# Kernel tuning notes

Hardware: AMD Instinct MI355X
Metric: run time of the kernel (lower is better)

Reference implementation:

```python
import jax, jax.numpy as jnp
import numpy as np

N_NODES = 50000
N_EDGES = 800000
IN_DIM = 128
OUT_DIM = 128
N_CLASSES = 10
N_GRAPHS = 64


def setup_inputs() -> dict:
    key = jax.random.key(0)
    ks = jax.random.split(key, 8)
    features = jax.random.normal(ks[0], (N_NODES, IN_DIM), dtype=jnp.float32)
    src = jax.random.randint(ks[1], (N_EDGES,), 0, N_NODES, dtype=jnp.int64)
    dst = jax.random.randint(ks[2], (N_EDGES,), 0, N_NODES, dtype=jnp.int64)
    graph_ids = jnp.sort(jax.random.randint(ks[3], (N_NODES,), 0, N_GRAPHS, dtype=jnp.int64))
    # GraphConv params (glorot-ish scale) and linear head params
    W = jax.random.normal(ks[4], (IN_DIM, OUT_DIM), dtype=jnp.float32) / np.sqrt(IN_DIM)
    b = jnp.zeros((OUT_DIM,), dtype=jnp.float32)
    W_head = jax.random.normal(ks[5], (OUT_DIM, N_CLASSES), dtype=jnp.float32) / np.sqrt(OUT_DIM)
    b_head = jnp.zeros((N_CLASSES,), dtype=jnp.float32)
    return {"features": features, "src": src, "dst": dst, "graph_ids": graph_ids,
            "W": W, "b": b, "W_head": W_head, "b_head": b_head}


def reference(features, src, dst, graph_ids, W, b, W_head, b_head):
    # DGL GraphConv, norm='both': D_out^-1/2 -> sum aggregate -> D_in^-1/2 -> XW+b -> relu
    ones_e = jnp.ones((src.shape[0],), dtype=features.dtype)
    out_deg = jax.ops.segment_sum(ones_e, src, num_segments=N_NODES)
    in_deg = jax.ops.segment_sum(ones_e, dst, num_segments=N_NODES)
    out_norm = jax.lax.rsqrt(jnp.clip(out_deg, 1.0))[:, None]   # [N,1]
    in_norm = jax.lax.rsqrt(jnp.clip(in_deg, 1.0))[:, None]     # [N,1]
    h = features * out_norm                                      # [N,D]
    agg = jax.ops.segment_sum(h[src], dst, num_segments=N_NODES) # gather-scatter [E,D]->[N,D]
    agg = agg * in_norm
    h = jax.nn.relu(agg @ W + b)                                 # [N,D_out]
    # dgl.mean_nodes: segment mean over graphs (note: original returns after layer 0)
    cnt = jax.ops.segment_sum(jnp.ones((N_NODES,), dtype=h.dtype), graph_ids, num_segments=N_GRAPHS)
    pooled = jax.ops.segment_sum(h, graph_ids, num_segments=N_GRAPHS) / jnp.clip(cnt, 1.0)[:, None]
    return pooled @ W_head + b_head                              # [G, n_classes]
```

## Files before the change

### kernel.cpp

```cpp
#include <hip/hip_runtime.h>

#define N_NODES   50000
#define N_EDGES   800000
#define DIM       128
#define N_GRAPHS  64
#define N_CLASSES 10
#define CAP       64
#define NCHE      64
#define CSZ       (N_EDGES / NCHE)
#define LQ        (N_NODES / 4)
#define WPB       64
#define NBR2      ((LQ + WPB - 1) / WPB)
#define PLACE_BPC ((CSZ + 255) / 256)
#define PLACE_BLKS (NCHE * PLACE_BPC)
#define PRES_BLKS ((N_NODES * DIM / 8 + 255) / 256)
#define K3_BLKS   (PLACE_BLKS + PRES_BLKS)
#define WT_BLKS   (DIM * DIM / 256)
#define GS_BLKS   ((N_NODES + 255) / 256)
#define LH_HIST   (2 * NCHE)
#define K1_BLKS   (LH_HIST + WT_BLKS + GS_BLKS)
#define NPBM      64
#define NBLK_NODE ((N_NODES + NPBM - 1) / NPBM)
#define WPAD      136

typedef _Float16 h8 __attribute__((ext_vector_type(8)));
typedef float f4v __attribute__((ext_vector_type(4)));

#define RSQN(D) rsqrtf(fmaxf((float)(D), 1.0f))

__global__ __launch_bounds__(256) void k_pre(const int* __restrict__ src,
                                             const int* __restrict__ dst,
                                             unsigned* __restrict__ Hin,
                                             unsigned* __restrict__ Hout,
                                             unsigned char* __restrict__ perm,
                                             const float* __restrict__ W,
                                             _Float16* __restrict__ Wt,
                                             const int* __restrict__ gid,
                                             int* __restrict__ gstart,
                                             const float* __restrict__ bh,
                                             float* __restrict__ out) {
    __shared__ unsigned L[LQ];
    int blk = blockIdx.x, t = threadIdx.x;
    if (blk >= LH_HIST) {
        int q = blk - LH_HIST;
        if (q < WT_BLKS) {
            int i = q * 256 + t;
            int n = i >> 7, k = i & 127;
            Wt[n * DIM + k] = (_Float16)W[k * DIM + n];
            if (i < N_GRAPHS * N_CLASSES) out[i] = bh[i % N_CLASSES];
        } else {
            int i = (q - WT_BLKS) * 256 + t;
            if (i < N_NODES) {
                int gq = gid[i];
                if (i == 0) {
                    for (int x = 0; x <= gq; ++x) gstart[x] = 0;
                } else {
                    int gp = gid[i - 1];
                    if (gp != gq)
                        for (int x = gp + 1; x <= gq; ++x) gstart[x] = i;
                }
                if (i == N_NODES - 1)
                    for (int x = gq + 1; x <= N_GRAPHS; ++x) gstart[x] = N_NODES;
            }
        }
        return;
    }
    int c = blk & (NCHE - 1);
    int phase = blk >> 6;
    int base = c * CSZ;
    for (int w = t; w < LQ; w += 256) L[w] = 0u;
    __syncthreads();
    if (phase == 0) {
        for (int i = t; i < CSZ; i += 256) {
            int d = dst[base + i];
            int sh = (d & 3) * 8;
            unsigned old = atomicAdd(&L[d >> 2], 1u << sh);
            perm[base + i] = (unsigned char)((old >> sh) & 0xffu);
        }
        __syncthreads();
        for (int w = t; w < LQ; w += 256) Hin[(size_t)c * LQ + w] = L[w];
    } else {
        for (int i = t; i < CSZ; i += 256) {
            int s = src[base + i];
            atomicAdd(&L[s >> 2], 1u << ((s & 3) * 8));
        }
        __syncthreads();
        for (int w = t; w < LQ; w += 256) Hout[(size_t)c * LQ + w] = L[w];
    }
}

__global__ __launch_bounds__(256) void k_reduce(unsigned* __restrict__ Hin,
                                                const unsigned* __restrict__ Hout,
                                                unsigned* __restrict__ indeg,
                                                unsigned* __restrict__ outdeg) {
    __shared__ unsigned sIn[4][WPB];
    __shared__ unsigned sOut[4][WPB];
    int t = threadIdx.x;
    int wl = t & (WPB - 1);
    int g  = t >> 6;
    int w  = blockIdx.x * WPB + wl;
    unsigned gs = 0, os = 0;
    int c0 = g * (NCHE / 4);
    if (w < LQ) {
        for (int c = c0; c < c0 + NCHE / 4; ++c) {
            gs += Hin[(size_t)c * LQ + w];
            os += Hout[(size_t)c * LQ + w];
        }
    }
    sIn[g][wl] = gs; sOut[g][wl] = os;
    __syncthreads();
    unsigned baseg = 0;
    for (int gg = 0; gg < 4; ++gg) if (gg < g) baseg += sIn[gg][wl];
    if (w < LQ) {
        unsigned running = baseg;
        for (int c = c0; c < c0 + NCHE / 4; ++c) {
            size_t idx = (size_t)c * LQ + w;
            unsigned word = Hin[idx];
            Hin[idx] = running;
            running += word;
        }
    }
    __syncthreads();
    if (t < WPB) {
        int ww = blockIdx.x * WPB + t;
        if (ww < LQ) {
            unsigned tot  = sIn[0][t] + sIn[1][t] + sIn[2][t] + sIn[3][t];
            unsigned otot = sOut[0][t] + sOut[1][t] + sOut[2][t] + sOut[3][t];
            int n = 4 * ww;
            indeg[n]      = tot & 0xffu;
            indeg[n + 1]  = (tot >> 8) & 0xffu;
            indeg[n + 2]  = (tot >> 16) & 0xffu;
            indeg[n + 3]  = tot >> 24;
            outdeg[n]     = otot & 0xffu;
            outdeg[n + 1] = (otot >> 8) & 0xffu;
            outdeg[n + 2] = (otot >> 16) & 0xffu;
            outdeg[n + 3] = otot >> 24;
        }
    }
}

__global__ __launch_bounds__(256) void k_place(const int* __restrict__ src,
                                               const int* __restrict__ dst,
                                               const unsigned* __restrict__ Hin,
                                               const unsigned char* __restrict__ perm,
                                               unsigned short* __restrict__ bsrc,
                                               const float* __restrict__ feat,
                                               const unsigned* __restrict__ outdeg,
                                               _Float16* __restrict__ sfeat) {
    int t = threadIdx.x;
    int blk = blockIdx.x;
    if (blk < PLACE_BLKS) {
        int c = blk / PLACE_BPC;
        int i = (blk % PLACE_BPC) * 256 + t;
        if (i < CSZ) {
            int e = c * CSZ + i;
            int d = dst[e];
            int sh = (d & 3) * 8;
            unsigned pre = (Hin[(size_t)c * LQ + (d >> 2)] >> sh) & 0xffu;
            unsigned slot = pre + perm[e];
            if (slot < CAP) bsrc[(size_t)d * CAP + slot] = (unsigned short)src[e];
        }
    } else {
        int i = (blk - PLACE_BLKS) * 256 + t;
        if (i < N_NODES * DIM / 8) {
            int n = i >> 4;
            float nrm = RSQN(outdeg[n]);
            const float4* p = reinterpret_cast<const float4*>(feat + (size_t)i * 8);
            float4 a = p[0], qv = p[1];
            h8 r;
            r[0] = (_Float16)(a.x * nrm);  r[1] = (_Float16)(a.y * nrm);
            r[2] = (_Float16)(a.z * nrm);  r[3] = (_Float16)(a.w * nrm);
            r[4] = (_Float16)(qv.x * nrm); r[5] = (_Float16)(qv.y * nrm);
            r[6] = (_Float16)(qv.z * nrm); r[7] = (_Float16)(qv.w * nrm);
            *reinterpret_cast<h8*>(sfeat + (size_t)i * 8) = r;
        }
    }
}

__device__ __forceinline__ h8 shfl_down_h8(h8 v, int d) {
    union { h8 h; int i[4]; } u;
    u.h = v;
    u.i[0] = __shfl_down(u.i[0], d);
    u.i[1] = __shfl_down(u.i[1], d);
    u.i[2] = __shfl_down(u.i[2], d);
    u.i[3] = __shfl_down(u.i[3], d);
    return u.h;
}

__global__ __launch_bounds__(256) void k_gather(const unsigned short* __restrict__ bsrc,
                                                const unsigned* __restrict__ indeg,
                                                const _Float16* __restrict__ sfeat,
                                                _Float16* __restrict__ aggh) {
    int tid = threadIdx.x;
    int wave = tid >> 6;
    int lane = tid & 63;
    int node = blockIdx.x * 4 + wave;
    if (node >= N_NODES) return;
    unsigned start = (unsigned)node * CAP;
    unsigned deg   = indeg[node];
    unsigned lim   = deg < (unsigned)CAP ? deg : (unsigned)CAP;
    int qtr = lane >> 4;
    int d8  = (lane & 15) << 3;
    int sIdx = 0;
    if ((unsigned)lane < lim) sIdx = bsrc[start + lane];
    h8 accA = (h8)(_Float16)0.f;
    h8 accC = (h8)(_Float16)0.f;
    for (unsigned j = 0; j < lim; j += 16) {
        unsigned j0 = j + qtr, j1 = j + 4 + qtr, j2 = j + 8 + qtr, j3 = j + 12 + qtr;
        int s0 = __shfl(sIdx, (int)(j0 < lim ? j0 : 0u));
        int s1 = __shfl(sIdx, (int)(j1 < lim ? j1 : 0u));
        int s2 = __shfl(sIdx, (int)(j2 < lim ? j2 : 0u));
        int s3 = __shfl(sIdx, (int)(j3 < lim ? j3 : 0u));
        _Float16 m0 = (j0 < lim) ? (_Float16)1.f : (_Float16)0.f;
        _Float16 m1 = (j1 < lim) ? (_Float16)1.f : (_Float16)0.f;
        _Float16 m2 = (j2 < lim) ? (_Float16)1.f : (_Float16)0.f;
        _Float16 m3 = (j3 < lim) ? (_Float16)1.f : (_Float16)0.f;
        h8 r0 = *reinterpret_cast<const h8*>(sfeat + (size_t)s0 * DIM + d8);
        h8 r1 = *reinterpret_cast<const h8*>(sfeat + (size_t)s1 * DIM + d8);
        h8 r2 = *reinterpret_cast<const h8*>(sfeat + (size_t)s2 * DIM + d8);
        h8 r3 = *reinterpret_cast<const h8*>(sfeat + (size_t)s3 * DIM + d8);
        accA += r0 * m0;
        accC += r1 * m1;
        accA += r2 * m2;
        accC += r3 * m3;
    }
    accA += accC;
    accA += shfl_down_h8(accA, 32);
    accA += shfl_down_h8(accA, 16);
    if (qtr == 0) {
        float innrm = RSQN(deg);
        h8 r;
#pragma unroll
        for (int k = 0; k < 8; ++k) r[k] = (_Float16)((float)accA[k] * innrm);
        *reinterpret_cast<h8*>(aggh + (size_t)node * DIM + d8) = r;
    }
}

__global__ __launch_bounds__(256) void k_node(const _Float16* __restrict__ aggh,
                                              const int* __restrict__ gid,
                                              const _Float16* __restrict__ Wt,
                                              const float* __restrict__ b,
                                              const float* __restrict__ Wh,
                                              const int* __restrict__ gstart,
                                              float* __restrict__ out) {
    __shared__ _Float16 Lw[DIM * WPAD];
    __shared__ float red[4][2][DIM];
    __shared__ float vb[2][DIM];
    int tid = threadIdx.x;
    int wave = tid >> 6, lane = tid & 63;
    int quad = lane >> 4, m = lane & 15;
    int blockBase = blockIdx.x * NPBM;
    int wbase = blockBase + wave * 16;
    int gfirst = gid[blockBase];
    int gsec = gfirst + 1;

    for (int i = tid; i < DIM * DIM / 8; i += 256) {
        int n = i >> 4, k8 = i & 15;
        h8 v = *reinterpret_cast<const h8*>(Wt + (size_t)n * DIM + k8 * 8);
        *reinterpret_cast<h8*>(&Lw[n * WPAD + k8 * 8]) = v;
    }
    __syncthreads();

    f4v acc[8];
#pragma unroll
    for (int t = 0; t < 8; ++t) acc[t] = (f4v){0,0,0,0};

#pragma unroll
    for (int kk = 0; kk < 4; ++kk) {
        int ko = kk * 32 + quad * 8;
        h8 a0 = *reinterpret_cast<const h8*>(aggh + (size_t)(wbase + m) * DIM + ko);
#pragma unroll
        for (int t = 0; t < 8; ++t) {
            h8 bf = *reinterpret_cast<const h8*>(&Lw[(t * 16 + m) * WPAD + ko]);
            acc[t] = __builtin_amdgcn_mfma_f32_16x16x32_f16(a0, bf, acc[t], 0, 0, 0);
        }
    }

    int n0 = wbase + quad * 4;
    float s0[8], s1[8];
#pragma unroll
    for (int t = 0; t < 8; ++t) {
        float bb = b[t * 16 + m];
        s0[t] = 0.f; s1[t] = 0.f;
        int dimIdx = t * 16 + m;
#pragma unroll
        for (int r = 0; r < 4; ++r) {
            int node = n0 + r;
            if (node < N_NODES) {
                float h = fmaxf(acc[t][r] + bb, 0.f);
                int g = gid[node];
                if (g == gfirst)      s0[t] += h;
                else if (g == gsec)   s1[t] += h;
                else {
                    float cntg = fmaxf((float)(gstart[g + 1] - gstart[g]), 1.f);
                    float hw = h / cntg;
                    for (int c = 0; c < N_CLASSES; ++c)
                        atomicAdd(&out[g * N_CLASSES + c], hw * Wh[dimIdx * N_CLASSES + c]);
                }
            }
        }
        s0[t] += __shfl_down(s0[t], 32);
        s0[t] += __shfl_down(s0[t], 16);
        s1[t] += __shfl_down(s1[t], 32);
        s1[t] += __shfl_down(s1[t], 16);
    }
    if (quad == 0) {
#pragma unroll
        for (int t = 0; t < 8; ++t) {
            red[wave][0][t * 16 + m] = s0[t];
            red[wave][1][t * 16 + m] = s1[t];
        }
    }
    __syncthreads();
    if (tid < DIM) {
        vb[0][tid] = red[0][0][tid] + red[1][0][tid] + red[2][0][tid] + red[3][0][tid];
        vb[1][tid] = red[0][1][tid] + red[1][1][tid] + red[2][1][tid] + red[3][1][tid];
    }
    __syncthreads();
    if (tid < N_CLASSES) {
        int c = tid;
        float s = 0.f;
#pragma unroll 8
        for (int k = 0; k < DIM; ++k) s += vb[0][k] * Wh[k * N_CLASSES + c];
        if (s != 0.f) {
            float cnt = fmaxf((float)(gstart[gfirst + 1] - gstart[gfirst]), 1.f);
            atomicAdd(&out[gfirst * N_CLASSES + c], s / cnt);
        }
    } else if (tid >= 64 && tid < 64 + N_CLASSES && gsec < N_GRAPHS) {
        int c = tid - 64;
        float s = 0.f;
#pragma unroll 8
        for (int k = 0; k < DIM; ++k) s += vb[1][k] * Wh[k * N_CLASSES + c];
        if (s != 0.f) {
            float cnt = fmaxf((float)(gstart[gsec + 1] - gstart[gsec]), 1.f);
            atomicAdd(&out[gsec * N_CLASSES + c], s / cnt);
        }
    }
}

extern "C" void kernel_launch(void* const* d_in, const int* in_sizes, int n_in,
                              void* d_out, int out_size, void* d_ws, size_t ws_size,
                              hipStream_t stream) {
    const float* feat = (const float*)d_in[0];
    const int*   src  = (const int*)d_in[1];
    const int*   dst  = (const int*)d_in[2];
    const int*   gid  = (const int*)d_in[3];
    const float* W    = (const float*)d_in[4];
    const float* b    = (const float*)d_in[5];
    const float* Wh   = (const float*)d_in[6];
    const float* bh   = (const float*)d_in[7];
    float* out = (float*)d_out;

    unsigned* indeg    = (unsigned*)d_ws;
    unsigned* outdeg   = indeg + N_NODES;
    int*      gstart   = (int*)(outdeg + N_NODES);
    unsigned short* bsrc = (unsigned short*)(gstart + 128);
    _Float16* sfeat    = (_Float16*)(bsrc + (size_t)N_NODES * CAP);
    _Float16* aggh     = sfeat + (size_t)N_NODES * DIM;
    _Float16* Wt       = aggh + (size_t)N_NODES * DIM;
    unsigned* Hin      = (unsigned*)(Wt + DIM * DIM);
    unsigned* Hout     = Hin + (size_t)NCHE * LQ;
    unsigned char* perm= (unsigned char*)(Hout + (size_t)NCHE * LQ);

    k_pre   <<<K1_BLKS, 256, 0, stream>>>(src, dst, Hin, Hout, perm,
                                          W, Wt, gid, gstart, bh, out);
    k_reduce<<<NBR2, 256, 0, stream>>>(Hin, Hout, indeg, outdeg);
    k_place <<<K3_BLKS, 256, 0, stream>>>(src, dst, Hin, perm, bsrc,
                                          feat, outdeg, sfeat);
    k_gather<<<(N_NODES + 3) / 4, 256, 0, stream>>>(bsrc, indeg, sfeat, aggh);
    k_node  <<<NBLK_NODE, 256, 0, stream>>>(aggh, gid, Wt, b, Wh, gstart, out);
}
```

Measured before the change: 159.2 us.

## Assign 16 lanes per node in gather, removing cross-quarter reduction

The gather kernel now maps each destination node to a 16-lane group instead of a full 64-lane wave. Each group walks all of its node's neighbors with a single accumulator, which removes the masked padding lanes and the shuffle reduction across quarters. Each thread now issues a serial chain of loads (average degree about 16), giving less memory-level parallelism per node. Wave-level divergence can also rise, because the four nodes in a wave have different degrees.

New measurement: 164.9 us. 1.04x slower.

```diff
diff --git a/kernel.cpp b/kernel.cpp
--- a/kernel.cpp
+++ b/kernel.cpp
@@ -22,6 +22,7 @@
 #define NPBM      64
 #define NBLK_NODE ((N_NODES + NPBM - 1) / NPBM)
 #define WPAD      136
+#define GQ_BLKS   ((N_NODES + 15) / 16)
 
 typedef _Float16 h8 __attribute__((ext_vector_type(8)));
 typedef float f4v __attribute__((ext_vector_type(4)));
@@ -177,63 +178,42 @@
     }
 }
 
-__device__ __forceinline__ h8 shfl_down_h8(h8 v, int d) {
-    union { h8 h; int i[4]; } u;
-    u.h = v;
-    u.i[0] = __shfl_down(u.i[0], d);
-    u.i[1] = __shfl_down(u.i[1], d);
-    u.i[2] = __shfl_down(u.i[2], d);
-    u.i[3] = __shfl_down(u.i[3], d);
-    return u.h;
-}
-
 __global__ __launch_bounds__(256) void k_gather(const unsigned short* __restrict__ bsrc,
                                                 const unsigned* __restrict__ indeg,
                                                 const _Float16* __restrict__ sfeat,
                                                 _Float16* __restrict__ aggh) {
     int tid = threadIdx.x;
-    int wave = tid >> 6;
-    int lane = tid & 63;
-    int node = blockIdx.x * 4 + wave;
+    int node = blockIdx.x * 16 + (tid >> 4);
     if (node >= N_NODES) return;
+    int l = tid & 15;
+    int qbase = (tid & 63) & 48;
     unsigned start = (unsigned)node * CAP;
-    unsigned deg   = indeg[node];
-    unsigned lim   = deg < (unsigned)CAP ? deg : (unsigned)CAP;
-    int qtr = lane >> 4;
-    int d8  = (lane & 15) << 3;
-    int sIdx = 0;
-    if ((unsigned)lane < lim) sIdx = bsrc[start + lane];
-    h8 accA = (h8)(_Float16)0.f;
-    h8 accC = (h8)(_Float16)0.f;
-    for (unsigned j = 0; j < lim; j += 16) {
-        unsigned j0 = j + qtr, j1 = j + 4 + qtr, j2 = j + 8 + qtr, j3 = j + 12 + qtr;
-        int s0 = __shfl(sIdx, (int)(j0 < lim ? j0 : 0u));
-        int s1 = __shfl(sIdx, (int)(j1 < lim ? j1 : 0u));
-        int s2 = __shfl(sIdx, (int)(j2 < lim ? j2 : 0u));
-        int s3 = __shfl(sIdx, (int)(j3 < lim ? j3 : 0u));
-        _Float16 m0 = (j0 < lim) ? (_Float16)1.f : (_Float16)0.f;
-        _Float16 m1 = (j1 < lim) ? (_Float16)1.f : (_Float16)0.f;
-        _Float16 m2 = (j2 < lim) ? (_Float16)1.f : (_Float16)0.f;
-        _Float16 m3 = (j3 < lim) ? (_Float16)1.f : (_Float16)0.f;
-        h8 r0 = *reinterpret_cast<const h8*>(sfeat + (size_t)s0 * DIM + d8);
-        h8 r1 = *reinterpret_cast<const h8*>(sfeat + (size_t)s1 * DIM + d8);
-        h8 r2 = *reinterpret_cast<const h8*>(sfeat + (size_t)s2 * DIM + d8);
-        h8 r3 = *reinterpret_cast<const h8*>(sfeat + (size_t)s3 * DIM + d8);
-        accA += r0 * m0;
-        accC += r1 * m1;
-        accA += r2 * m2;
-        accC += r3 * m3;
-    }
-    accA += accC;
-    accA += shfl_down_h8(accA, 32);
-    accA += shfl_down_h8(accA, 16);
-    if (qtr == 0) {
-        float innrm = RSQN(deg);
-        h8 r;
-#pragma unroll
-        for (int k = 0; k < 8; ++k) r[k] = (_Float16)((float)accA[k] * innrm);
-        *reinterpret_cast<h8*>(aggh + (size_t)node * DIM + d8) = r;
-    }
+    unsigned deg = indeg[node];
+    unsigned lim = deg < (unsigned)CAP ? deg : (unsigned)CAP;
+    int d8 = l << 3;
+    h8 acc = (h8)(_Float16)0.f;
+    unsigned full = lim & ~15u;
+    for (unsigned j0 = 0; j0 < full; j0 += 16) {
+        int myIdx = bsrc[start + j0 + (unsigned)l];
+#pragma unroll
+        for (int jj = 0; jj < 16; ++jj) {
+            int s = __shfl(myIdx, qbase + jj);
+            acc += *reinterpret_cast<const h8*>(sfeat + (size_t)s * DIM + d8);
+        }
+    }
+    unsigned rem = lim - full;
+    if (rem) {
+        int myIdx = bsrc[start + full + (unsigned)l];
+        for (unsigned jj = 0; jj < rem; ++jj) {
+            int s = __shfl(myIdx, qbase + (int)jj);
+            acc += *reinterpret_cast<const h8*>(sfeat + (size_t)s * DIM + d8);
+        }
+    }
+    float innrm = RSQN(deg);
+    h8 r;
+#pragma unroll
+    for (int k = 0; k < 8; ++k) r[k] = (_Float16)((float)acc[k] * innrm);
+    *reinterpret_cast<h8*>(aggh + (size_t)node * DIM + d8) = r;
 }
 
 __global__ __launch_bounds__(256) void k_node(const _Float16* __restrict__ aggh,
@@ -367,6 +347,6 @@
     k_reduce<<<NBR2, 256, 0, stream>>>(Hin, Hout, indeg, outdeg);
     k_place <<<K3_BLKS, 256, 0, stream>>>(src, dst, Hin, perm, bsrc,
                                           feat, outdeg, sfeat);
-    k_gather<<<(N_NODES + 3) / 4, 256, 0, stream>>>(bsrc, indeg, sfeat, aggh);
+    k_gather<<<GQ_BLKS, 256, 0, stream>>>(bsrc, indeg, sfeat, aggh);
     k_node  <<<NBLK_NODE, 256, 0, stream>>>(aggh, gid, Wt, b, Wh, gstart, out);
 }
```
